# Kernel optimization log

Measured on AMD Instinct MI355X. Metric: run time of the kernel, lower is better.

Reference implementation:

```python
import jax, jax.numpy as jnp
import numpy as np

B, N, DIM, H = 8, 1024, 512, 8
D = DIM // H
SCALE = DIM ** -0.5


def setup_inputs() -> dict:
    key = jax.random.key(0)
    ks = jax.random.split(key, 8)
    s = 0.02
    return {
        "x": jax.random.normal(ks[0], (B, N, DIM), dtype=jnp.float32),
        "mask": jax.random.uniform(ks[1], (1, 1, N, N), dtype=jnp.float32),
        "Wqkv1": jax.random.normal(ks[2], (DIM, 3 * DIM), dtype=jnp.float32) * s,
        "bqkv1": jnp.zeros((3 * DIM,), dtype=jnp.float32),
        "Wqkv2": jax.random.normal(ks[3], (DIM, 3 * DIM), dtype=jnp.float32) * s,
        "bqkv2": jnp.zeros((3 * DIM,), dtype=jnp.float32),
        "Wnn1": jax.random.normal(ks[4], (DIM, DIM), dtype=jnp.float32) * s,
        "bnn1": jnp.zeros((DIM,), dtype=jnp.float32),
    }


def _split_heads(qkv, b, n):
    # qkv: [b, n, 3*dim] -> three [b, h, n, d]
    q, k, v = jnp.split(qkv, 3, axis=-1)
    r = lambda t: t.reshape(b, n, H, D).transpose(0, 2, 1, 3)
    return r(q), r(k), r(v)


def reference(x, mask, Wqkv1, bqkv1, Wqkv2, bqkv2, Wnn1, bnn1):
    b, n, dim = x.shape
    # Stage 1: mask-scaled sigmoid attention (no softmax, no scale)
    q, k, v = _split_heads(x @ Wqkv1 + bqkv1, b, n)
    dots = jax.nn.sigmoid(jnp.einsum('bhid,bhjd->bhij', q, k) * mask)
    out1 = jnp.einsum('bhij,bhjd->bhid', dots, v)
    out1 = out1.transpose(0, 2, 1, 3).reshape(b, n, dim)
    # Stage 2: standard scaled softmax attention on stage-1 output
    q, k, v = _split_heads(out1 @ Wqkv2 + bqkv2, b, n)
    attn = jax.nn.softmax(jnp.einsum('bhid,bhjd->bhij', q, k) * SCALE, axis=-1)
    out = jnp.einsum('bhij,bhjd->bhid', attn, v)
    out = out.transpose(0, 2, 1, 3).reshape(b, n, dim)
    # Output projection (dropout is identity in eval mode)
    return out @ Wnn1 + bnn1
```

## Files before the change

kernel.cpp:

```cpp
#include <hip/hip_runtime.h>
#include <hip/hip_bf16.h>
#include <stdint.h>

constexpr int B_ = 8, N_ = 1024, DIM_ = 512, H_ = 8, D_ = 64;
constexpr int BH_ = B_ * H_;
constexpr int M_  = B_ * N_;
constexpr float SCALE_ = 0.04419417382415922f;
constexpr float LOG2E_ = 1.44269504088896f;
constexpr float QSL2E_ = SCALE_ * LOG2E_;

typedef __bf16 bf16x8 __attribute__((ext_vector_type(8)));
typedef float  f32x4  __attribute__((ext_vector_type(4)));
typedef unsigned short u16;
typedef u16 u16x8 __attribute__((ext_vector_type(8)));
typedef u16 u16x4 __attribute__((ext_vector_type(4)));

static __device__ __forceinline__ u16 f2bf(float f) {
  return __builtin_bit_cast(u16, (__bf16)f);
}
static __device__ __forceinline__ bf16x8 ld8(const u16* p) {
  return __builtin_bit_cast(bf16x8, *reinterpret_cast<const u16x8*>(p));
}
static __device__ __forceinline__ f32x4 mfma16(bf16x8 a, bf16x8 b, f32x4 c) {
  return __builtin_amdgcn_mfma_f32_16x16x32_bf16(a, b, c, 0, 0, 0);
}
static __device__ __forceinline__ void gload_lds16(const u16* g, void* l) {
  __builtin_amdgcn_global_load_lds(
      (const __attribute__((address_space(1))) void*)g,
      (__attribute__((address_space(3))) void*)l, 16, 0, 0);
}

__global__ void k_cvt(const float* __restrict__ in, u16* __restrict__ out, int n4) {
  int i = blockIdx.x * blockDim.x + threadIdx.x;
  int stride = gridDim.x * blockDim.x;
  for (int idx = i; idx < n4; idx += stride) {
    float4 v = reinterpret_cast<const float4*>(in)[idx];
    u16x4 o;
    o[0] = f2bf(v.x); o[1] = f2bf(v.y); o[2] = f2bf(v.z); o[3] = f2bf(v.w);
    reinterpret_cast<u16x4*>(out)[idx] = o;
  }
}

__global__ void k_mask(const float* __restrict__ in, float* __restrict__ out, int n4) {
  int i = blockIdx.x * blockDim.x + threadIdx.x;
  int stride = gridDim.x * blockDim.x;
  for (int idx = i; idx < n4; idx += stride) {
    float4 v = reinterpret_cast<const float4*>(in)[idx];
    v.x *= -LOG2E_; v.y *= -LOG2E_; v.z *= -LOG2E_; v.w *= -LOG2E_;
    reinterpret_cast<float4*>(out)[idx] = v;
  }
}

__global__ void k_wt(const float* __restrict__ W, u16* __restrict__ Wt, int ncols, float qs) {
  int idx = blockIdx.x * 256 + threadIdx.x;
  if (idx >= ncols * 512) return;
  int c = idx >> 9, k = idx & 511;
  float v = W[k * ncols + c];
  if (c < 512) v *= qs;
  Wt[idx] = f2bf(v);
}

template<int NC, int MODE, bool SQ>
__global__ __launch_bounds__(256) void k_gemm(
    const u16* __restrict__ A, const u16* __restrict__ Wt, const float* __restrict__ bias,
    u16* __restrict__ qo, u16* __restrict__ ko, u16* __restrict__ vto, float* __restrict__ fo)
{
  __shared__ __attribute__((aligned(16))) u16 As[2][128 * 32];
  __shared__ __attribute__((aligned(16))) u16 Bs[2][128 * 32];
  const int wv = threadIdx.x >> 6, ln = threadIdx.x & 63;
  const int lr = ln & 15, lg = ln >> 4;
  const int wr = wv >> 1, wc = wv & 1;
  const int r0 = blockIdx.x * 128;
  const int c0 = blockIdx.y * 128;

  auto stage = [&](int bufi, int kk) {
#pragma unroll
    for (int q = 0; q < 2; ++q) {
      int L = (wv * 2 + q) * 1024 + ln * 16;
      int row = L >> 6;
      int col = ((L & 63) ^ (((row >> 1) & 3) << 4)) >> 1;
      gload_lds16(A  + (size_t)(r0 + row) * 512 + kk + col, (char*)As[bufi] + (wv * 2 + q) * 1024);
      gload_lds16(Wt + (size_t)(c0 + row) * 512 + kk + col, (char*)Bs[bufi] + (wv * 2 + q) * 1024);
    }
  };
  auto swzld = [&](const u16* tile, int row, int colb) -> bf16x8 {
    int byte = (row << 6) + (colb ^ (((row >> 1) & 3) << 4));
    return __builtin_bit_cast(bf16x8, *reinterpret_cast<const u16x8*>((const char*)tile + byte));
  };

  f32x4 acc[4][4] = {};
  stage(0, 0);
  int buf = 0;
  for (int kk = 0; kk < 512; kk += 32) {
    __syncthreads();
    if (kk + 32 < 512) stage(buf ^ 1, kk + 32);
    bf16x8 af[4], bfb[4];
#pragma unroll
    for (int m = 0; m < 4; ++m) af[m]  = swzld(As[buf], wr * 64 + m * 16 + lr, lg * 16);
#pragma unroll
    for (int n = 0; n < 4; ++n) bfb[n] = swzld(Bs[buf], wc * 64 + n * 16 + lr, lg * 16);
#pragma unroll
    for (int m = 0; m < 4; ++m)
#pragma unroll
      for (int n = 0; n < 4; ++n)
        acc[m][n] = mfma16(af[m], bfb[n], acc[m][n]);
    buf ^= 1;
  }

#pragma unroll
  for (int m = 0; m < 4; ++m)
#pragma unroll
    for (int n = 0; n < 4; ++n) {
      const int gc  = c0 + wc * 64 + n * 16 + lr;
      const int gr0 = r0 + wr * 64 + m * 16 + lg * 4;
      const float bsc = (SQ && gc < 512) ? QSL2E_ : 1.f;
      const float bv = bias[gc] * bsc;
      if (MODE == 0) {
        const int part = gc >> 9, cc = gc & 511;
        const int hh = cc >> 6, dd = cc & 63;
        const int bb = gr0 >> 10, nn = gr0 & 1023;
        const int bh = bb * H_ + hh;
        if (part == 2) {
          u16x4 w;
#pragma unroll
          for (int r = 0; r < 4; ++r) w[r] = f2bf(acc[m][n][r] + bv);
          *reinterpret_cast<u16x4*>(&vto[((size_t)(bh * D_ + dd)) * N_ + nn]) = w;
        } else {
          u16* dst = (part == 0 ? qo : ko) + ((size_t)(bh * N_ + nn)) * D_ + dd;
#pragma unroll
          for (int r = 0; r < 4; ++r) dst[(size_t)r * D_] = f2bf(acc[m][n][r] + bv);
        }
      } else {
#pragma unroll
        for (int r = 0; r < 4; ++r)
          fo[(size_t)(gr0 + r) * NC + gc] = acc[m][n][r] + bv;
      }
    }
}

template<int STAGE>
__global__ __launch_bounds__(512, 4) void k_attn(
    const u16* __restrict__ Q, const u16* __restrict__ K, const u16* __restrict__ Vt,
    const float* __restrict__ mask, u16* __restrict__ O)
{
  __shared__ __attribute__((aligned(16))) u16 Kb[2][64 * 64];
  __shared__ __attribute__((aligned(16))) u16 Vb[2][64 * 64];
  __shared__ __attribute__((aligned(16))) u16 pbuf[8][16][72];
  const int wv = threadIdx.x >> 6, ln = threadIdx.x & 63;
  const int lr = ln & 15, lg = ln >> 4;
  const int bh = blockIdx.y;
  const int i0 = blockIdx.x * 128 + wv * 16;
  const size_t base = (size_t)bh * N_ * D_;

  auto stageKV = [&](int bufi, int jt2) {
    int L = wv * 1024 + ln * 16;
    int row = L >> 7;
    int col = ((L & 127) ^ ((row & 7) << 4)) >> 1;
    gload_lds16(K  + base + (size_t)(jt2 + row) * 64 + col,  (char*)Kb[bufi] + wv * 1024);
    gload_lds16(Vt + base + (size_t)row * 1024 + jt2 + col,  (char*)Vb[bufi] + wv * 1024);
  };
  auto swzld = [&](const u16* tile, int row, int colb) -> bf16x8 {
    int byte = (row << 7) + (colb ^ ((row & 7) << 4));
    return __builtin_bit_cast(bf16x8, *reinterpret_cast<const u16x8*>((const char*)tile + byte));
  };

  bf16x8 aq0 = ld8(Q + base + (size_t)(i0 + lr) * D_ + lg * 8);
  bf16x8 aq1 = ld8(Q + base + (size_t)(i0 + lr) * D_ + 32 + lg * 8);

  f32x4 acco[4] = {};
  float ssum_ln = 0.f;

  float4 mk[4];
  const float* mrow = mask + (size_t)(i0 + lr) * N_;
  auto loadmask = [&](int jt2) {
#pragma unroll
    for (int js = 0; js < 4; ++js)
      mk[js] = *reinterpret_cast<const float4*>(&mrow[jt2 + js * 16 + lg * 4]);
  };
  if (STAGE == 1) loadmask(0);

  stageKV(0, 0);
  int buf = 0;
  for (int jt = 0; jt < N_; jt += 64) {
    __syncthreads();
    if (jt + 64 < N_) stageKV(buf ^ 1, jt + 64);

    f32x4 s[4];
    __builtin_amdgcn_s_setprio(1);
#pragma unroll
    for (int js = 0; js < 4; ++js) {
      int krow = js * 16 + lr;
      bf16x8 bk0 = swzld(Kb[buf], krow, lg * 16);
      bf16x8 bk1 = swzld(Kb[buf], krow, 64 + lg * 16);
      f32x4 z = {};
      z = mfma16(bk0, aq0, z);
      z = mfma16(bk1, aq1, z);
      s[js] = z;
    }
    __builtin_amdgcn_s_setprio(0);

    if (STAGE == 1) {
#pragma unroll
      for (int js = 0; js < 4; ++js) {
        u16x4 w;
#pragma unroll
        for (int r = 0; r < 4; ++r) {
          float mkr = (r == 0) ? mk[js].x : (r == 1) ? mk[js].y : (r == 2) ? mk[js].z : mk[js].w;
          float e = exp2f(s[js][r] * mkr);
          w[r] = f2bf(__builtin_amdgcn_rcpf(1.f + e));
        }
        *reinterpret_cast<u16x4*>(&pbuf[wv][lr][js * 16 + lg * 4]) = w;
      }
      if (jt + 64 < N_) loadmask(jt + 64);
    } else {
      float ps = 0.f;
#pragma unroll
      for (int js = 0; js < 4; ++js) {
        u16x4 w;
#pragma unroll
        for (int r = 0; r < 4; ++r) {
          float p = exp2f(s[js][r]);
          ps += p;
          w[r] = f2bf(p);
        }
        *reinterpret_cast<u16x4*>(&pbuf[wv][lr][js * 16 + lg * 4]) = w;
      }
      ssum_ln += ps;
    }

    bf16x8 ap0 = ld8(&pbuf[wv][lr][lg * 8]);
    bf16x8 ap1 = ld8(&pbuf[wv][lr][32 + lg * 8]);
    __builtin_amdgcn_s_setprio(1);
#pragma unroll
    for (int db = 0; db < 4; ++db) {
      bf16x8 bv0 = swzld(Vb[buf], db * 16 + lr, lg * 16);
      bf16x8 bv1 = swzld(Vb[buf], db * 16 + lr, 64 + lg * 16);
      acco[db] = mfma16(ap1, bv1, mfma16(ap0, bv0, acco[db]));
    }
    __builtin_amdgcn_s_setprio(0);
    buf ^= 1;
  }

  float inv[4];
  if (STAGE == 2) {
    float st = ssum_ln;
    st += __shfl_xor(st, 16);
    st += __shfl_xor(st, 32);
#pragma unroll
    for (int r = 0; r < 4; ++r)
      inv[r] = __builtin_amdgcn_rcpf(__shfl(st, lg * 4 + r));
  }

#pragma unroll
  for (int db = 0; db < 4; ++db)
#pragma unroll
    for (int r = 0; r < 4; ++r) {
      float v = acco[db][r];
      if (STAGE == 2) v *= inv[r];
      pbuf[wv][lg * 4 + r][db * 16 + lr] = f2bf(v);
    }
  bf16x8 o0v = ld8(&pbuf[wv][lr][lg * 8]);
  bf16x8 o1v = ld8(&pbuf[wv][lr][32 + lg * 8]);
  const int bb = bh >> 3, hh = bh & 7;
  u16* orow = O + (size_t)(bb * N_ + i0 + lr) * DIM_ + hh * D_;
  *reinterpret_cast<u16x8*>(orow + lg * 8)      = __builtin_bit_cast(u16x8, o0v);
  *reinterpret_cast<u16x8*>(orow + 32 + lg * 8) = __builtin_bit_cast(u16x8, o1v);
}

extern "C" void kernel_launch(void* const* d_in, const int* in_sizes, int n_in,
                              void* d_out, int out_size, void* d_ws, size_t ws_size,
                              hipStream_t stream)
{
  const float* x    = (const float*)d_in[0];
  const float* mask = (const float*)d_in[1];
  const float* W1   = (const float*)d_in[2];
  const float* b1   = (const float*)d_in[3];
  const float* W2   = (const float*)d_in[4];
  const float* b2   = (const float*)d_in[5];
  const float* W3   = (const float*)d_in[6];
  const float* b3   = (const float*)d_in[7];
  float* out = (float*)d_out;

  char* ws = (char*)d_ws;
  size_t off = 0;
  auto alloc = [&](size_t bytes) { char* p = ws + off; off += (bytes + 255) & ~255ULL; return p; };
  u16*   W1t = (u16*)alloc((size_t)1536 * 512 * 2);
  u16*   W2t = (u16*)alloc((size_t)1536 * 512 * 2);
  u16*   W3t = (u16*)alloc((size_t)512 * 512 * 2);
  u16*   xb  = (u16*)alloc((size_t)M_ * DIM_ * 2);
  u16*   q   = (u16*)alloc((size_t)BH_ * N_ * D_ * 2);
  u16*   k   = (u16*)alloc((size_t)BH_ * N_ * D_ * 2);
  u16*   vt  = (u16*)alloc((size_t)BH_ * N_ * D_ * 2);
  u16*   o1  = (u16*)alloc((size_t)M_ * DIM_ * 2);
  float* mk  = (float*)alloc((size_t)N_ * N_ * 4);
  u16*   o2  = xb;

  k_cvt<<<2048, 256, 0, stream>>>(x, xb, M_ * DIM_ / 4);
  k_mask<<<1024, 256, 0, stream>>>(mask, mk, N_ * N_ / 4);
  k_wt<<<(1536 * 512 + 255) / 256, 256, 0, stream>>>(W1, W1t, 1536, 1.f);
  k_wt<<<(1536 * 512 + 255) / 256, 256, 0, stream>>>(W2, W2t, 1536, QSL2E_);
  k_wt<<<(512 * 512 + 255) / 256, 256, 0, stream>>>(W3, W3t, 512, 1.f);

  dim3 g1(M_ / 128, 1536 / 128);
  k_gemm<1536, 0, false><<<g1, 256, 0, stream>>>(xb, W1t, b1, q, k, vt, nullptr);

  dim3 ga(N_ / 128, BH_);
  k_attn<1><<<ga, 512, 0, stream>>>(q, k, vt, mk, o1);

  k_gemm<1536, 0, true><<<g1, 256, 0, stream>>>(o1, W2t, b2, q, k, vt, nullptr);

  k_attn<2><<<ga, 512, 0, stream>>>(q, k, vt, mk, o2);

  dim3 g3(M_ / 128, 512 / 128);
  k_gemm<512, 1, false><<<g3, 256, 0, stream>>>(o2, W3t, b3, nullptr, nullptr, nullptr, out);
}
```

Baseline: 228.5 us.

## Fuse prep kernels, swizzle workgroup order, drop LDS staging in attention

Merges the five preprocessing launches into one k_prep kernel that dispatches on block index. Both the GEMM and the attention kernels now remap workgroup IDs so neighbouring workgroups share tiles in L2. The attention kernel drops LDS double-buffering of K/V and the barriers, reading K and V fragments straight from global memory into registers, and halves the block to 256 threads with 64 query rows each. This removes launch overhead and synchronisation but duplicates K/V global traffic across waves and gives up explicit load/compute overlap. The GEMM swizzle hardcodes 64 row tiles, which holds for both the 1536-column and 512-column grids.

```diff
diff --git a/kernel.cpp b/kernel.cpp
--- a/kernel.cpp
+++ b/kernel.cpp
@@ -30,34 +30,38 @@
       (__attribute__((address_space(3))) void*)l, 16, 0, 0);
 }
 
-__global__ void k_cvt(const float* __restrict__ in, u16* __restrict__ out, int n4) {
-  int i = blockIdx.x * blockDim.x + threadIdx.x;
-  int stride = gridDim.x * blockDim.x;
-  for (int idx = i; idx < n4; idx += stride) {
-    float4 v = reinterpret_cast<const float4*>(in)[idx];
-    u16x4 o;
-    o[0] = f2bf(v.x); o[1] = f2bf(v.y); o[2] = f2bf(v.z); o[3] = f2bf(v.w);
-    reinterpret_cast<u16x4*>(out)[idx] = o;
+__global__ void k_prep(const float* __restrict__ x, const float* __restrict__ mask,
+                       const float* __restrict__ W1, const float* __restrict__ W2,
+                       const float* __restrict__ W3,
+                       u16* __restrict__ xb, float* __restrict__ mk,
+                       u16* __restrict__ W1t, u16* __restrict__ W2t, u16* __restrict__ W3t)
+{
+  const int b = blockIdx.x, t = threadIdx.x;
+  if (b < 4096) {
+    int idx = b * 256 + t;
+    float4 v = reinterpret_cast<const float4*>(x)[idx];
+    u16x4 o; o[0] = f2bf(v.x); o[1] = f2bf(v.y); o[2] = f2bf(v.z); o[3] = f2bf(v.w);
+    reinterpret_cast<u16x4*>(xb)[idx] = o;
+  } else if (b < 5120) {
+    int idx = (b - 4096) * 256 + t;
+    float4 v = reinterpret_cast<const float4*>(mask)[idx];
+    v.x *= -LOG2E_; v.y *= -LOG2E_; v.z *= -LOG2E_; v.w *= -LOG2E_;
+    reinterpret_cast<float4*>(mk)[idx] = v;
+  } else if (b < 8192) {
+    int idx = (b - 5120) * 256 + t;
+    int c = idx >> 9, k = idx & 511;
+    W1t[idx] = f2bf(W1[k * 1536 + c]);
+  } else if (b < 11264) {
+    int idx = (b - 8192) * 256 + t;
+    int c = idx >> 9, k = idx & 511;
+    float v = W2[k * 1536 + c];
+    if (c < 512) v *= QSL2E_;
+    W2t[idx] = f2bf(v);
+  } else {
+    int idx = (b - 11264) * 256 + t;
+    int c = idx >> 9, k = idx & 511;
+    W3t[idx] = f2bf(W3[k * 512 + c]);
   }
-}
-
-__global__ void k_mask(const float* __restrict__ in, float* __restrict__ out, int n4) {
-  int i = blockIdx.x * blockDim.x + threadIdx.x;
-  int stride = gridDim.x * blockDim.x;
-  for (int idx = i; idx < n4; idx += stride) {
-    float4 v = reinterpret_cast<const float4*>(in)[idx];
-    v.x *= -LOG2E_; v.y *= -LOG2E_; v.z *= -LOG2E_; v.w *= -LOG2E_;
-    reinterpret_cast<float4*>(out)[idx] = v;
-  }
-}
-
-__global__ void k_wt(const float* __restrict__ W, u16* __restrict__ Wt, int ncols, float qs) {
-  int idx = blockIdx.x * 256 + threadIdx.x;
-  if (idx >= ncols * 512) return;
-  int c = idx >> 9, k = idx & 511;
-  float v = W[k * ncols + c];
-  if (c < 512) v *= qs;
-  Wt[idx] = f2bf(v);
 }
 
 template<int NC, int MODE, bool SQ>
@@ -70,8 +74,11 @@
   const int wv = threadIdx.x >> 6, ln = threadIdx.x & 63;
   const int lr = ln & 15, lg = ln >> 4;
   const int wr = wv >> 1, wc = wv & 1;
-  const int r0 = blockIdx.x * 128;
-  const int c0 = blockIdx.y * 128;
+  const int nwg = gridDim.x * gridDim.y;
+  const int lin = blockIdx.y * gridDim.x + blockIdx.x;
+  const int swz = (lin & 7) * (nwg >> 3) + (lin >> 3);
+  const int r0 = (swz & 63) * 128;
+  const int c0 = (swz >> 6) * 128;
 
   auto stage = [&](int bufi, int kk) {
 #pragma unroll
@@ -139,30 +146,20 @@
 }
 
 template<int STAGE>
-__global__ __launch_bounds__(512, 4) void k_attn(
+__global__ __launch_bounds__(256, 4) void k_attn(
     const u16* __restrict__ Q, const u16* __restrict__ K, const u16* __restrict__ Vt,
     const float* __restrict__ mask, u16* __restrict__ O)
 {
-  __shared__ __attribute__((aligned(16))) u16 Kb[2][64 * 64];
-  __shared__ __attribute__((aligned(16))) u16 Vb[2][64 * 64];
-  __shared__ __attribute__((aligned(16))) u16 pbuf[8][16][72];
+  __shared__ __attribute__((aligned(16))) u16 pbuf[4][16][72];
   const int wv = threadIdx.x >> 6, ln = threadIdx.x & 63;
   const int lr = ln & 15, lg = ln >> 4;
-  const int bh = blockIdx.y;
-  const int i0 = blockIdx.x * 128 + wv * 16;
+  const int lin = blockIdx.y * 16 + blockIdx.x;
+  const int swz = (lin & 7) * 128 + (lin >> 3);
+  const int bh = swz >> 4;
+  const int i0 = (swz & 15) * 64 + wv * 16;
   const size_t base = (size_t)bh * N_ * D_;
-
-  auto stageKV = [&](int bufi, int jt2) {
-    int L = wv * 1024 + ln * 16;
-    int row = L >> 7;
-    int col = ((L & 127) ^ ((row & 7) << 4)) >> 1;
-    gload_lds16(K  + base + (size_t)(jt2 + row) * 64 + col,  (char*)Kb[bufi] + wv * 1024);
-    gload_lds16(Vt + base + (size_t)row * 1024 + jt2 + col,  (char*)Vb[bufi] + wv * 1024);
-  };
-  auto swzld = [&](const u16* tile, int row, int colb) -> bf16x8 {
-    int byte = (row << 7) + (colb ^ ((row & 7) << 4));
-    return __builtin_bit_cast(bf16x8, *reinterpret_cast<const u16x8*>((const char*)tile + byte));
-  };
+  const u16* Kp = K + base;
+  const u16* Vp = Vt + base;
 
   bf16x8 aq0 = ld8(Q + base + (size_t)(i0 + lr) * D_ + lg * 8);
   bf16x8 aq1 = ld8(Q + base + (size_t)(i0 + lr) * D_ + 32 + lg * 8);
@@ -179,25 +176,23 @@
   };
   if (STAGE == 1) loadmask(0);
 
-  stageKV(0, 0);
-  int buf = 0;
   for (int jt = 0; jt < N_; jt += 64) {
-    __syncthreads();
-    if (jt + 64 < N_) stageKV(buf ^ 1, jt + 64);
+    bf16x8 bk0[4], bk1[4];
+#pragma unroll
+    for (int js = 0; js < 4; ++js) {
+      const u16* kp = Kp + (size_t)(jt + js * 16 + lr) * D_;
+      bk0[js] = ld8(kp + lg * 8);
+      bk1[js] = ld8(kp + 32 + lg * 8);
+    }
 
     f32x4 s[4];
-    __builtin_amdgcn_s_setprio(1);
 #pragma unroll
     for (int js = 0; js < 4; ++js) {
-      int krow = js * 16 + lr;
-      bf16x8 bk0 = swzld(Kb[buf], krow, lg * 16);
-      bf16x8 bk1 = swzld(Kb[buf], krow, 64 + lg * 16);
       f32x4 z = {};
-      z = mfma16(bk0, aq0, z);
-      z = mfma16(bk1, aq1, z);
+      z = mfma16(bk0[js], aq0, z);
+      z = mfma16(bk1[js], aq1, z);
       s[js] = z;
     }
-    __builtin_amdgcn_s_setprio(0);
 
     if (STAGE == 1) {
 #pragma unroll
@@ -230,15 +225,13 @@
 
     bf16x8 ap0 = ld8(&pbuf[wv][lr][lg * 8]);
     bf16x8 ap1 = ld8(&pbuf[wv][lr][32 + lg * 8]);
-    __builtin_amdgcn_s_setprio(1);
 #pragma unroll
     for (int db = 0; db < 4; ++db) {
-      bf16x8 bv0 = swzld(Vb[buf], db * 16 + lr, lg * 16);
-      bf16x8 bv1 = swzld(Vb[buf], db * 16 + lr, 64 + lg * 16);
+      const u16* vp = Vp + (size_t)(db * 16 + lr) * N_ + jt;
+      bf16x8 bv0 = ld8(vp + lg * 8);
+      bf16x8 bv1 = ld8(vp + 32 + lg * 8);
       acco[db] = mfma16(ap1, bv1, mfma16(ap0, bv0, acco[db]));
     }
-    __builtin_amdgcn_s_setprio(0);
-    buf ^= 1;
   }
 
   float inv[4];
@@ -295,21 +288,17 @@
   float* mk  = (float*)alloc((size_t)N_ * N_ * 4);
   u16*   o2  = xb;
 
-  k_cvt<<<2048, 256, 0, stream>>>(x, xb, M_ * DIM_ / 4);
-  k_mask<<<1024, 256, 0, stream>>>(mask, mk, N_ * N_ / 4);
-  k_wt<<<(1536 * 512 + 255) / 256, 256, 0, stream>>>(W1, W1t, 1536, 1.f);
-  k_wt<<<(1536 * 512 + 255) / 256, 256, 0, stream>>>(W2, W2t, 1536, QSL2E_);
-  k_wt<<<(512 * 512 + 255) / 256, 256, 0, stream>>>(W3, W3t, 512, 1.f);
+  k_prep<<<12288, 256, 0, stream>>>(x, mask, W1, W2, W3, xb, mk, W1t, W2t, W3t);
 
   dim3 g1(M_ / 128, 1536 / 128);
   k_gemm<1536, 0, false><<<g1, 256, 0, stream>>>(xb, W1t, b1, q, k, vt, nullptr);
 
-  dim3 ga(N_ / 128, BH_);
-  k_attn<1><<<ga, 512, 0, stream>>>(q, k, vt, mk, o1);
+  dim3 ga(16, BH_);
+  k_attn<1><<<ga, 256, 0, stream>>>(q, k, vt, mk, o1);
 
   k_gemm<1536, 0, true><<<g1, 256, 0, stream>>>(o1, W2t, b2, q, k, vt, nullptr);
 
-  k_attn<2><<<ga, 512, 0, stream>>>(q, k, vt, mk, o2);
+  k_attn<2><<<ga, 256, 0, stream>>>(q, k, vt, mk, o2);
 
   dim3 g3(M_ / 128, 512 / 128);
   k_gemm<512, 1, false><<<g3, 256, 0, stream>>>(o2, W3t, b3, nullptr, nullptr, nullptr, out);
```

Result: slower. 409.4 us (+79.2%).
